# Kernel optimization log

Hardware: AMD Instinct MI355X
Metric: run time of the kernel (lower is better)

## Reference

```python
import jax, jax.numpy as jnp
import numpy as np

B, C, D, H, W = 2, 256, 4, 32, 32


def setup_inputs() -> dict:
    key = jax.random.key(0)
    k1, k2, k3, k4, k5 = jax.random.split(key, 5)
    s = 1.0 / np.sqrt(C)
    return {
        "exemplar_features": jax.random.normal(k1, (B, C, D, H, W), jnp.float32),
        "query_features": jax.random.normal(k2, (B, C, D, H, W), jnp.float32),
        "W_ex": jax.random.normal(k3, (C, C), jnp.float32) * s,    # nn.Linear weight (out,in)
        "W_q": jax.random.normal(k4, (C, C), jnp.float32) * s,     # nn.Linear weight (out,in)
        "W_gate": jax.random.normal(k5, (1, C, 1, 1, 1), jnp.float32) * s,  # Conv3d 1x1x1 weight
    }


def reference(exemplar_features, query_features, W_ex, W_q, W_gate):
    b, c, d, h, w = query_features.shape
    n = d * h * w
    ex = exemplar_features.reshape(b, c, n)   # (B,C,N)
    q = query_features.reshape(b, c, n)       # (B,C,N)
    ex_t = jnp.swapaxes(ex, 1, 2)              # (B,N,C)
    q_t = jnp.swapaxes(q, 1, 2)                # (B,N,C)
    # nn.Linear(no bias): x @ W.T
    ex_corr = jnp.einsum('bnc,dc->bnd', ex_t, W_ex)   # (B,N,C)
    q_corr = jnp.einsum('bnc,dc->bnd', q_t, W_q)      # (B,N,C)
    corr_e2q = jnp.einsum('bnc,bcm->bnm', ex_corr, q)  # (B,N,N)
    corr_q2e = jnp.einsum('bnc,bcm->bnm', q_corr, ex)  # (B,N,N)
    # softmax(transpose(corr,1,2), dim=1)
    A_e2q = jax.nn.softmax(jnp.swapaxes(corr_e2q, 1, 2), axis=1)  # (B,N,N)
    A_q2e = jax.nn.softmax(jnp.swapaxes(corr_q2e, 1, 2), axis=1)  # (B,N,N)
    ex_att = jnp.einsum('bcn,bnm->bcm', ex, A_e2q).reshape(b, c, d, h, w)
    q_att = jnp.einsum('bcn,bnm->bcm', q, A_q2e).reshape(b, c, d, h, w)
    # 1x1x1 Conv3d (256 -> 1, no bias) is a channel contraction
    g = W_gate[:, :, 0, 0, 0]  # (1,C)
    ex_mask = jax.nn.sigmoid(jnp.einsum('oc,bcdhw->bodhw', g, ex_att))
    q_mask = jax.nn.sigmoid(jnp.einsum('oc,bcdhw->bodhw', g, q_att))
    return ex_mask, q_mask, A_e2q, A_q2e
```

## Files before the change

kernel.cpp:

```cpp
#include <hip/hip_runtime.h>
#include <math.h>

#define BSZ  2
#define CDIM 256
#define NDIM 4096
#define SHIFT 110.0f

typedef _Float16 f16;
typedef f16  f16x8 __attribute__((ext_vector_type(8)));
typedef float f32x4 __attribute__((ext_vector_type(4)));

static const size_t F16N   = (size_t)BSZ * NDIM * CDIM;
static const size_t WS_FB  = 3 * F16N / 2;

__device__ __forceinline__ void gl_lds16(const void* g, void* l) {
    __builtin_amdgcn_global_load_lds(
        (const __attribute__((address_space(1))) void*)g,
        (__attribute__((address_space(3))) void*)l, 16, 0, 0);
}

__global__ __launch_bounds__(256) void corr_kernel(
    const float* __restrict__ ex, const float* __restrict__ q,
    const float* __restrict__ W_ex, const float* __restrict__ W_q,
    f16* __restrict__ Ah_e, f16* __restrict__ Al_e,
    f16* __restrict__ Ah_q, f16* __restrict__ Al_q)
{
    const int z   = blockIdx.z;
    const int sel = z >> 1;
    const int b   = z & 1;
    const float* feat = sel ? q   : ex;
    const float* W    = sel ? W_q : W_ex;
    f16* Ah = sel ? Ah_q : Ah_e;
    f16* Al = sel ? Al_q : Al_e;

    const int m0  = blockIdx.x * 128;
    const int cc0 = blockIdx.y * 128;
    const int t   = threadIdx.x;
    const int tx  = t & 15;
    const int ty  = t >> 4;

    __shared__ float sA[8][128];
    __shared__ float sB[8][128];

    float acc[8][8];
#pragma unroll
    for (int i = 0; i < 8; i++)
#pragma unroll
        for (int j = 0; j < 8; j++) acc[i][j] = 0.f;

    for (int k0 = 0; k0 < CDIM; k0 += 8) {
        {
            int kk = t >> 5, mi = (t & 31) * 4;
            *(float4*)(&sA[kk][mi]) =
                *(const float4*)(feat + ((size_t)(b * CDIM + k0 + kk)) * NDIM + m0 + mi);
        }
        {
            int ccj = t >> 1, kkb = (t & 1) * 4;
            float4 f = *(const float4*)(W + (size_t)(cc0 + ccj) * CDIM + k0 + kkb);
            sB[kkb + 0][ccj] = f.x; sB[kkb + 1][ccj] = f.y;
            sB[kkb + 2][ccj] = f.z; sB[kkb + 3][ccj] = f.w;
        }
        __syncthreads();
#pragma unroll
        for (int kk = 0; kk < 8; kk++) {
            float a[8], bb[8];
            *(float4*)(a)      = *(const float4*)(&sA[kk][ty * 8]);
            *(float4*)(a + 4)  = *(const float4*)(&sA[kk][ty * 8 + 4]);
            *(float4*)(bb)     = *(const float4*)(&sB[kk][tx * 8]);
            *(float4*)(bb + 4) = *(const float4*)(&sB[kk][tx * 8 + 4]);
#pragma unroll
            for (int i = 0; i < 8; i++)
#pragma unroll
                for (int j = 0; j < 8; j++)
                    acc[i][j] = fmaf(a[i], bb[j], acc[i][j]);
        }
        __syncthreads();
    }
#pragma unroll
    for (int i = 0; i < 8; i++) {
        const int m = m0 + ty * 8 + i;
        f16x8 hv, lv;
#pragma unroll
        for (int j = 0; j < 8; j++) {
            float x = acc[i][j];
            f16 hh = (f16)x;
            hv[j] = hh;
            lv[j] = (f16)(x - (float)hh);
        }
        const size_t off = ((size_t)(b * NDIM + m)) * CDIM + cc0 + tx * 8;
        *(f16x8*)(Ah + off) = hv;
        *(f16x8*)(Al + off) = lv;
    }
}

__global__ __launch_bounds__(256) void pack_b_kernel(
    const float* __restrict__ ex, const float* __restrict__ q,
    f16* __restrict__ Bq, f16* __restrict__ Bex)
{
    const int z   = blockIdx.z;
    const int sel = z >> 1;
    const int b   = z & 1;
    const float* feat = sel ? ex : q;
    f16* outp         = sel ? Bex : Bq;

    const int n0 = blockIdx.x * 64, c0 = blockIdx.y * 64;
    __shared__ float sT[64][65];
    const int t = threadIdx.x;
    const int tn = t & 63, tr = t >> 6;
#pragma unroll
    for (int r = 0; r < 16; ++r) {
        int c = tr + r * 4;
        sT[c][tn] = feat[((size_t)(b * CDIM + c0 + c)) * NDIM + n0 + tn];
    }
    __syncthreads();
#pragma unroll
    for (int r = 0; r < 16; ++r) {
        int n = tr + r * 4;
        outp[((size_t)(b * NDIM + n0 + n)) * CDIM + c0 + tn] = (f16)sT[tn][n];
    }
}

__global__ __launch_bounds__(256) void v_kernel(
    const float* __restrict__ ex, const float* __restrict__ q,
    const float* __restrict__ g,
    float* __restrict__ v_ex, float* __restrict__ v_q)
{
    __shared__ float sg[CDIM];
    const int t = threadIdx.x;
    sg[t] = g[t];
    __syncthreads();

    const int sel = blockIdx.z;
    const int b   = blockIdx.y;
    const float* feat = sel ? q : ex;
    float* outp       = sel ? v_q : v_ex;

    const int n = blockIdx.x * 256 + t;
    float acc = 0.f;
    for (int c = 0; c < CDIM; c++)
        acc = fmaf(sg[c], feat[((size_t)(b * CDIM + c)) * NDIM + n], acc);
    outp[b * NDIM + n] = acc;
}

__global__ __launch_bounds__(256) void score_mfma_kernel(
    const f16* __restrict__ Ah, const f16* __restrict__ Al,
    const f16* __restrict__ Bp, const float* __restrict__ v,
    float* __restrict__ outU,
    float* __restrict__ rowsum, float* __restrict__ rowdot)
{
    const int bb = blockIdx.z;
    const int m0 = blockIdx.x * 128;
    const int n0 = blockIdx.y * 128;
    const int t    = threadIdx.x;
    const int lane = t & 63;
    const int wv   = t >> 6;
    const int lq   = lane >> 4;
    const int ll   = lane & 15;

    __shared__ f16 sAh[8][128][8];
    __shared__ f16 sAl[8][128][8];
    __shared__ f16 sB [8][128][8];

    f32x4 acc[2][8];
#pragma unroll
    for (int mf = 0; mf < 2; mf++)
#pragma unroll
        for (int nf = 0; nf < 8; nf++) acc[mf][nf] = (f32x4)0.f;

    for (int k0 = 0; k0 < CDIM; k0 += 64) {
        if (k0) __syncthreads();
#pragma unroll
        for (int it = 0; it < 4; ++it) {
            const int cidx = (wv * 4 + it) * 64 + lane;
            const int kb = cidx >> 7;
            const int rr = cidx & 127;
            const size_t gA = ((size_t)(bb * NDIM + m0 + rr)) * CDIM + k0 + kb * 8;
            const size_t gB = ((size_t)(bb * NDIM + n0 + rr)) * CDIM + k0 + kb * 8;
            gl_lds16(Ah + gA, (char*)sAh + (size_t)cidx * 16);
            gl_lds16(Al + gA, (char*)sAl + (size_t)cidx * 16);
            gl_lds16(Bp + gB, (char*)sB  + (size_t)cidx * 16);
        }
        __syncthreads();
#pragma unroll
        for (int s = 0; s < 2; ++s) {
            f16x8 bfr[8];
#pragma unroll
            for (int nf = 0; nf < 8; ++nf)
                bfr[nf] = *(const f16x8*)&sB[4 * s + lq][nf * 16 + ll][0];
#pragma unroll
            for (int mf = 0; mf < 2; ++mf) {
                f16x8 ah = *(const f16x8*)&sAh[4 * s + lq][wv * 32 + mf * 16 + ll][0];
                f16x8 al = *(const f16x8*)&sAl[4 * s + lq][wv * 32 + mf * 16 + ll][0];
#pragma unroll
                for (int nf = 0; nf < 8; ++nf) {
                    acc[mf][nf] = __builtin_amdgcn_mfma_f32_16x16x32_f16(ah, bfr[nf], acc[mf][nf], 0, 0, 0);
                    acc[mf][nf] = __builtin_amdgcn_mfma_f32_16x16x32_f16(al, bfr[nf], acc[mf][nf], 0, 0, 0);
                }
            }
        }
    }

    float vv[8];
#pragma unroll
    for (int nf = 0; nf < 8; ++nf) vv[nf] = v[bb * NDIM + n0 + nf * 16 + ll];

    float rs[2][4], rd[2][4];
#pragma unroll
    for (int mf = 0; mf < 2; mf++)
#pragma unroll
        for (int r = 0; r < 4; r++) { rs[mf][r] = 0.f; rd[mf][r] = 0.f; }

#pragma unroll
    for (int mf = 0; mf < 2; ++mf) {
        const int mbase = m0 + wv * 32 + mf * 16 + lq * 4;
#pragma unroll
        for (int nf = 0; nf < 8; ++nf) {
            const int n = n0 + nf * 16 + ll;
            float4 u;
            u.x = __expf(acc[mf][nf][0] - SHIFT);
            u.y = __expf(acc[mf][nf][1] - SHIFT);
            u.z = __expf(acc[mf][nf][2] - SHIFT);
            u.w = __expf(acc[mf][nf][3] - SHIFT);
            *(float4*)(outU + ((size_t)(bb * NDIM + n)) * NDIM + mbase) = u;
            rs[mf][0] += u.x; rs[mf][1] += u.y; rs[mf][2] += u.z; rs[mf][3] += u.w;
            rd[mf][0] += u.x * vv[nf]; rd[mf][1] += u.y * vv[nf];
            rd[mf][2] += u.z * vv[nf]; rd[mf][3] += u.w * vv[nf];
        }
    }
#pragma unroll
    for (int mf = 0; mf < 2; ++mf) {
#pragma unroll
        for (int r = 0; r < 4; ++r) {
#pragma unroll
            for (int off = 1; off < 16; off <<= 1) {
                rs[mf][r] += __shfl_xor(rs[mf][r], off);
                rd[mf][r] += __shfl_xor(rd[mf][r], off);
            }
        }
        if (ll == 0) {
            const int mbase = m0 + wv * 32 + mf * 16 + lq * 4;
#pragma unroll
            for (int r = 0; r < 4; ++r) {
                atomicAdd(rowsum + bb * NDIM + mbase + r, rs[mf][r]);
                atomicAdd(rowdot + bb * NDIM + mbase + r, rd[mf][r]);
            }
        }
    }
}

__global__ __launch_bounds__(256) void mask_kernel(
    const float* __restrict__ sum_e, const float* __restrict__ dot_e,
    const float* __restrict__ sum_q, const float* __restrict__ dot_q,
    float* __restrict__ inv_e, float* __restrict__ inv_q,
    float* __restrict__ outp)
{
    const int idx = blockIdx.x * 256 + threadIdx.x;
    const int j = idx >> 13, i = idx & 8191;
    const float* s = j ? sum_q : sum_e;
    const float* d = j ? dot_q : dot_e;
    float* inv     = j ? inv_q : inv_e;
    const float sv = s[i];
    const float iv = 1.0f / sv;
    inv[i] = iv;
    const float x = d[i] * iv;
    outp[idx] = 1.0f / (1.0f + __expf(-x));
}

__global__ __launch_bounds__(256) void rescale_kernel(
    float* __restrict__ A, const float* __restrict__ inv)
{
    const size_t total4 = (size_t)BSZ * NDIM * NDIM / 4;
    const size_t stride = (size_t)gridDim.x * 256;
    for (size_t i4 = (size_t)blockIdx.x * 256 + threadIdx.x; i4 < total4; i4 += stride) {
        const size_t f = i4 * 4;
        const int m = (int)(f & (NDIM - 1));
        const int b = (int)(f >> 24);
        float4 u  = *(float4*)(A + f);
        float4 iv = *(const float4*)(inv + b * NDIM + m);
        u.x *= iv.x; u.y *= iv.y; u.z *= iv.z; u.w *= iv.w;
        *(float4*)(A + f) = u;
    }
}

extern "C" void kernel_launch(void* const* d_in, const int* in_sizes, int n_in,
                              void* d_out, int out_size, void* d_ws, size_t ws_size,
                              hipStream_t stream)
{
    const float* ex   = (const float*)d_in[0];
    const float* q    = (const float*)d_in[1];
    const float* W_ex = (const float*)d_in[2];
    const float* W_q  = (const float*)d_in[3];
    const float* g    = (const float*)d_in[4];
    float* outp = (float*)d_out;

    float* A_e2q = outp + 16384;
    float* A_q2e = A_e2q + (size_t)BSZ * NDIM * NDIM;

    f16* Ah_e = (f16*)A_q2e;
    f16* Al_e = Ah_e + F16N;
    f16* Bq   = Al_e + F16N;

    f16* Ah_q = (f16*)d_ws;
    f16* Al_q = Ah_q + F16N;
    f16* Bex  = Al_q + F16N;
    float* wsf  = (float*)d_ws + WS_FB;
    float* v_ex = wsf;
    float* v_q  = wsf + 8192;
    float* sum_e = wsf + 2 * 8192;
    float* dot_e = wsf + 3 * 8192;
    float* sum_q = wsf + 4 * 8192;
    float* dot_q = wsf + 5 * 8192;
    float* inv_e = wsf + 6 * 8192;
    float* inv_q = wsf + 7 * 8192;

    hipMemsetAsync(sum_e, 0, 4 * 8192 * sizeof(float), stream);

    corr_kernel<<<dim3(NDIM / 128, CDIM / 128, 2 * BSZ), 256, 0, stream>>>(
        ex, q, W_ex, W_q, Ah_e, Al_e, Ah_q, Al_q);

    pack_b_kernel<<<dim3(NDIM / 64, CDIM / 64, 2 * BSZ), 256, 0, stream>>>(
        ex, q, Bq, Bex);

    v_kernel<<<dim3(NDIM / 256, BSZ, 2), 256, 0, stream>>>(ex, q, g, v_ex, v_q);

    score_mfma_kernel<<<dim3(32, 32, BSZ), 256, 0, stream>>>(
        Ah_e, Al_e, Bq, v_ex, A_e2q, sum_e, dot_e);
    score_mfma_kernel<<<dim3(32, 32, BSZ), 256, 0, stream>>>(
        Ah_q, Al_q, Bex, v_q, A_q2e, sum_q, dot_q);

    mask_kernel<<<64, 256, 0, stream>>>(sum_e, dot_e, sum_q, dot_q, inv_e, inv_q, outp);

    rescale_kernel<<<32768, 256, 0, stream>>>(A_e2q, inv_e);
    rescale_kernel<<<32768, 256, 0, stream>>>(A_q2e, inv_q);
}
```

Baseline: 562.6 us.

## Fuse softmax normalization into score kernel via two-pass recompute

Replaces the tiled score GEMM plus atomics, mask kernel and two full-matrix rescale passes with one kernel per direction. Each block owns 16 rows: a first pass computes row sums and gate dot products, and a second pass recomputes the scores and writes normalized probabilities directly. This removes a full read-modify-write of both 128MB attention matrices, the memset and the atomics. In exchange it doubles the MFMA work and loads operands straight from global memory into registers instead of staging them in LDS, on a grid of only 512 blocks.

```diff
diff --git a/kernel.cpp b/kernel.cpp
--- a/kernel.cpp
+++ b/kernel.cpp
@@ -12,12 +12,6 @@
 
 static const size_t F16N   = (size_t)BSZ * NDIM * CDIM;
 static const size_t WS_FB  = 3 * F16N / 2;
-
-__device__ __forceinline__ void gl_lds16(const void* g, void* l) {
-    __builtin_amdgcn_global_load_lds(
-        (const __attribute__((address_space(1))) void*)g,
-        (__attribute__((address_space(3))) void*)l, 16, 0, 0);
-}
 
 __global__ __launch_bounds__(256) void corr_kernel(
     const float* __restrict__ ex, const float* __restrict__ q,
@@ -142,144 +136,131 @@
     outp[b * NDIM + n] = acc;
 }
 
-__global__ __launch_bounds__(256) void score_mfma_kernel(
+__global__ __launch_bounds__(256, 2) void flash_score_kernel(
     const f16* __restrict__ Ah, const f16* __restrict__ Al,
     const f16* __restrict__ Bp, const float* __restrict__ v,
-    float* __restrict__ outU,
-    float* __restrict__ rowsum, float* __restrict__ rowdot)
-{
-    const int bb = blockIdx.z;
-    const int m0 = blockIdx.x * 128;
-    const int n0 = blockIdx.y * 128;
-    const int t    = threadIdx.x;
-    const int lane = t & 63;
-    const int wv   = t >> 6;
-    const int lq   = lane >> 4;
-    const int ll   = lane & 15;
-
-    __shared__ f16 sAh[8][128][8];
-    __shared__ f16 sAl[8][128][8];
-    __shared__ f16 sB [8][128][8];
-
-    f32x4 acc[2][8];
-#pragma unroll
-    for (int mf = 0; mf < 2; mf++)
-#pragma unroll
-        for (int nf = 0; nf < 8; nf++) acc[mf][nf] = (f32x4)0.f;
-
-    for (int k0 = 0; k0 < CDIM; k0 += 64) {
-        if (k0) __syncthreads();
-#pragma unroll
-        for (int it = 0; it < 4; ++it) {
-            const int cidx = (wv * 4 + it) * 64 + lane;
-            const int kb = cidx >> 7;
-            const int rr = cidx & 127;
-            const size_t gA = ((size_t)(bb * NDIM + m0 + rr)) * CDIM + k0 + kb * 8;
-            const size_t gB = ((size_t)(bb * NDIM + n0 + rr)) * CDIM + k0 + kb * 8;
-            gl_lds16(Ah + gA, (char*)sAh + (size_t)cidx * 16);
-            gl_lds16(Al + gA, (char*)sAl + (size_t)cidx * 16);
-            gl_lds16(Bp + gB, (char*)sB  + (size_t)cidx * 16);
-        }
-        __syncthreads();
-#pragma unroll
-        for (int s = 0; s < 2; ++s) {
-            f16x8 bfr[8];
-#pragma unroll
-            for (int nf = 0; nf < 8; ++nf)
-                bfr[nf] = *(const f16x8*)&sB[4 * s + lq][nf * 16 + ll][0];
-#pragma unroll
-            for (int mf = 0; mf < 2; ++mf) {
-                f16x8 ah = *(const f16x8*)&sAh[4 * s + lq][wv * 32 + mf * 16 + ll][0];
-                f16x8 al = *(const f16x8*)&sAl[4 * s + lq][wv * 32 + mf * 16 + ll][0];
-#pragma unroll
-                for (int nf = 0; nf < 8; ++nf) {
-                    acc[mf][nf] = __builtin_amdgcn_mfma_f32_16x16x32_f16(ah, bfr[nf], acc[mf][nf], 0, 0, 0);
-                    acc[mf][nf] = __builtin_amdgcn_mfma_f32_16x16x32_f16(al, bfr[nf], acc[mf][nf], 0, 0, 0);
-                }
-            }
-        }
-    }
-
-    float vv[8];
-#pragma unroll
-    for (int nf = 0; nf < 8; ++nf) vv[nf] = v[bb * NDIM + n0 + nf * 16 + ll];
-
-    float rs[2][4], rd[2][4];
-#pragma unroll
-    for (int mf = 0; mf < 2; mf++)
-#pragma unroll
-        for (int r = 0; r < 4; r++) { rs[mf][r] = 0.f; rd[mf][r] = 0.f; }
-
-#pragma unroll
-    for (int mf = 0; mf < 2; ++mf) {
-        const int mbase = m0 + wv * 32 + mf * 16 + lq * 4;
-#pragma unroll
-        for (int nf = 0; nf < 8; ++nf) {
-            const int n = n0 + nf * 16 + ll;
-            float4 u;
-            u.x = __expf(acc[mf][nf][0] - SHIFT);
-            u.y = __expf(acc[mf][nf][1] - SHIFT);
-            u.z = __expf(acc[mf][nf][2] - SHIFT);
-            u.w = __expf(acc[mf][nf][3] - SHIFT);
-            *(float4*)(outU + ((size_t)(bb * NDIM + n)) * NDIM + mbase) = u;
-            rs[mf][0] += u.x; rs[mf][1] += u.y; rs[mf][2] += u.z; rs[mf][3] += u.w;
-            rd[mf][0] += u.x * vv[nf]; rd[mf][1] += u.y * vv[nf];
-            rd[mf][2] += u.z * vv[nf]; rd[mf][3] += u.w * vv[nf];
-        }
-    }
-#pragma unroll
-    for (int mf = 0; mf < 2; ++mf) {
+    float* __restrict__ outA, float* __restrict__ outMask)
+{
+    const int bb = blockIdx.y;
+    const int x  = blockIdx.x;
+    const int gpair = ((x >> 4) << 3) + (x & 7);
+    const int m0 = (gpair * 2 + ((x >> 3) & 1)) * 16;
+
+    const int t = threadIdx.x, lane = t & 63, wv = t >> 6;
+    const int lq = lane >> 4, ll = lane & 15;
+
+    const size_t aoff = ((size_t)(bb * NDIM + m0 + ll)) * CDIM + lq * 8;
+    f16x8 ah[8], al[8];
+#pragma unroll
+    for (int s = 0; s < 8; ++s) {
+        ah[s] = *(const f16x8*)(Ah + aoff + s * 32);
+        al[s] = *(const f16x8*)(Al + aoff + s * 32);
+    }
+
+    const f16*   bpw = Bp + ((size_t)(bb * NDIM + wv * 1024 + ll)) * CDIM + lq * 8;
+    const float* vp  = v + bb * NDIM + wv * 1024 + ll;
+    float*       outw = outA + ((size_t)(bb * NDIM + wv * 1024 + ll)) * NDIM + m0 + lq * 4;
+
+    f16x8 bx[16], by[16];
+    float rs[4] = {0.f, 0.f, 0.f, 0.f}, rd[4] = {0.f, 0.f, 0.f, 0.f};
+    float iv[4];
+
+#define LOADP(buf_, nf_) do {                                                 \
+        const f16* _p0 = bpw + (size_t)(nf_) * 16 * CDIM;                     \
+        const f16* _p1 = _p0 + 16 * CDIM;                                     \
+        _Pragma("unroll")                                                     \
+        for (int _s = 0; _s < 8; ++_s) {                                      \
+            buf_[_s]     = *(const f16x8*)(_p0 + _s * 32);                    \
+            buf_[8 + _s] = *(const f16x8*)(_p1 + _s * 32);                    \
+        } } while (0)
+
+#define MF(buf_, a0_, a1_) do {                                               \
+        _Pragma("unroll")                                                     \
+        for (int _s = 0; _s < 8; ++_s) {                                      \
+            a0_ = __builtin_amdgcn_mfma_f32_16x16x32_f16(ah[_s], buf_[_s],     a0_, 0, 0, 0); \
+            a0_ = __builtin_amdgcn_mfma_f32_16x16x32_f16(al[_s], buf_[_s],     a0_, 0, 0, 0); \
+            a1_ = __builtin_amdgcn_mfma_f32_16x16x32_f16(ah[_s], buf_[8 + _s], a1_, 0, 0, 0); \
+            a1_ = __builtin_amdgcn_mfma_f32_16x16x32_f16(al[_s], buf_[8 + _s], a1_, 0, 0, 0); \
+        } } while (0)
+
+#define CSUM(buf_, nf_) do {                                                  \
+        f32x4 _a0 = (f32x4)0.f, _a1 = (f32x4)0.f;                             \
+        MF(buf_, _a0, _a1);                                                   \
+        const float _v0 = vp[(nf_) * 16], _v1 = vp[(nf_) * 16 + 16];          \
+        _Pragma("unroll")                                                     \
+        for (int _r = 0; _r < 4; ++_r) {                                      \
+            const float _u0 = __expf(_a0[_r] - SHIFT);                        \
+            const float _u1 = __expf(_a1[_r] - SHIFT);                        \
+            rs[_r] += _u0 + _u1;                                              \
+            rd[_r] += _u0 * _v0 + _u1 * _v1;                                  \
+        } } while (0)
+
+#define CST(buf_, nf_) do {                                                   \
+        f32x4 _a0 = (f32x4)0.f, _a1 = (f32x4)0.f;                             \
+        MF(buf_, _a0, _a1);                                                   \
+        float4 _u;                                                            \
+        _u.x = __expf(_a0[0] - SHIFT) * iv[0];                                \
+        _u.y = __expf(_a0[1] - SHIFT) * iv[1];                                \
+        _u.z = __expf(_a0[2] - SHIFT) * iv[2];                                \
+        _u.w = __expf(_a0[3] - SHIFT) * iv[3];                                \
+        *(float4*)(outw + (size_t)(nf_) * 16 * NDIM) = _u;                    \
+        _u.x = __expf(_a1[0] - SHIFT) * iv[0];                                \
+        _u.y = __expf(_a1[1] - SHIFT) * iv[1];                                \
+        _u.z = __expf(_a1[2] - SHIFT) * iv[2];                                \
+        _u.w = __expf(_a1[3] - SHIFT) * iv[3];                                \
+        *(float4*)(outw + (size_t)(nf_ + 1) * 16 * NDIM) = _u;                \
+    } while (0)
+
+    LOADP(bx, 0);
+#pragma unroll 1
+    for (int nf = 0; nf < 64; nf += 4) {
+        LOADP(by, nf + 2);
+        CSUM(bx, nf);
+        if (nf + 4 < 64) LOADP(bx, nf + 4);
+        CSUM(by, nf + 2);
+    }
+
+#pragma unroll
+    for (int r = 0; r < 4; ++r)
+#pragma unroll
+        for (int off = 1; off < 16; off <<= 1) {
+            rs[r] += __shfl_xor(rs[r], off);
+            rd[r] += __shfl_xor(rd[r], off);
+        }
+
+    __shared__ float redS[4][4][4], redD[4][4][4];
+    if (ll == 0)
+#pragma unroll
+        for (int r = 0; r < 4; ++r) { redS[wv][lq][r] = rs[r]; redD[wv][lq][r] = rd[r]; }
+    __syncthreads();
+
+#pragma unroll
+    for (int r = 0; r < 4; ++r) {
+        const float ssum = redS[0][lq][r] + redS[1][lq][r] + redS[2][lq][r] + redS[3][lq][r];
+        iv[r] = 1.0f / ssum;
+    }
+    if (wv == 0 && ll == 0) {
 #pragma unroll
         for (int r = 0; r < 4; ++r) {
-#pragma unroll
-            for (int off = 1; off < 16; off <<= 1) {
-                rs[mf][r] += __shfl_xor(rs[mf][r], off);
-                rd[mf][r] += __shfl_xor(rd[mf][r], off);
-            }
-        }
-        if (ll == 0) {
-            const int mbase = m0 + wv * 32 + mf * 16 + lq * 4;
-#pragma unroll
-            for (int r = 0; r < 4; ++r) {
-                atomicAdd(rowsum + bb * NDIM + mbase + r, rs[mf][r]);
-                atomicAdd(rowdot + bb * NDIM + mbase + r, rd[mf][r]);
-            }
-        }
-    }
-}
-
-__global__ __launch_bounds__(256) void mask_kernel(
-    const float* __restrict__ sum_e, const float* __restrict__ dot_e,
-    const float* __restrict__ sum_q, const float* __restrict__ dot_q,
-    float* __restrict__ inv_e, float* __restrict__ inv_q,
-    float* __restrict__ outp)
-{
-    const int idx = blockIdx.x * 256 + threadIdx.x;
-    const int j = idx >> 13, i = idx & 8191;
-    const float* s = j ? sum_q : sum_e;
-    const float* d = j ? dot_q : dot_e;
-    float* inv     = j ? inv_q : inv_e;
-    const float sv = s[i];
-    const float iv = 1.0f / sv;
-    inv[i] = iv;
-    const float x = d[i] * iv;
-    outp[idx] = 1.0f / (1.0f + __expf(-x));
-}
-
-__global__ __launch_bounds__(256) void rescale_kernel(
-    float* __restrict__ A, const float* __restrict__ inv)
-{
-    const size_t total4 = (size_t)BSZ * NDIM * NDIM / 4;
-    const size_t stride = (size_t)gridDim.x * 256;
-    for (size_t i4 = (size_t)blockIdx.x * 256 + threadIdx.x; i4 < total4; i4 += stride) {
-        const size_t f = i4 * 4;
-        const int m = (int)(f & (NDIM - 1));
-        const int b = (int)(f >> 24);
-        float4 u  = *(float4*)(A + f);
-        float4 iv = *(const float4*)(inv + b * NDIM + m);
-        u.x *= iv.x; u.y *= iv.y; u.z *= iv.z; u.w *= iv.w;
-        *(float4*)(A + f) = u;
-    }
+            const float dsum = redD[0][lq][r] + redD[1][lq][r] + redD[2][lq][r] + redD[3][lq][r];
+            const float xx = dsum * iv[r];
+            outMask[bb * NDIM + m0 + lq * 4 + r] = 1.0f / (1.0f + __expf(-xx));
+        }
+    }
+
+    LOADP(bx, 0);
+#pragma unroll 1
+    for (int nf = 0; nf < 64; nf += 4) {
+        LOADP(by, nf + 2);
+        CST(bx, nf);
+        if (nf + 4 < 64) LOADP(bx, nf + 4);
+        CST(by, nf + 2);
+    }
+
+#undef LOADP
+#undef MF
+#undef CSUM
+#undef CST
 }
 
 extern "C" void kernel_launch(void* const* d_in, const int* in_sizes, int n_in,
@@ -306,14 +287,6 @@
     float* wsf  = (float*)d_ws + WS_FB;
     float* v_ex = wsf;
     float* v_q  = wsf + 8192;
-    float* sum_e = wsf + 2 * 8192;
-    float* dot_e = wsf + 3 * 8192;
-    float* sum_q = wsf + 4 * 8192;
-    float* dot_q = wsf + 5 * 8192;
-    float* inv_e = wsf + 6 * 8192;
-    float* inv_q = wsf + 7 * 8192;
-
-    hipMemsetAsync(sum_e, 0, 4 * 8192 * sizeof(float), stream);
 
     corr_kernel<<<dim3(NDIM / 128, CDIM / 128, 2 * BSZ), 256, 0, stream>>>(
         ex, q, W_ex, W_q, Ah_e, Al_e, Ah_q, Al_q);
@@ -323,13 +296,8 @@
 
     v_kernel<<<dim3(NDIM / 256, BSZ, 2), 256, 0, stream>>>(ex, q, g, v_ex, v_q);
 
-    score_mfma_kernel<<<dim3(32, 32, BSZ), 256, 0, stream>>>(
-        Ah_e, Al_e, Bq, v_ex, A_e2q, sum_e, dot_e);
-    score_mfma_kernel<<<dim3(32, 32, BSZ), 256, 0, stream>>>(
-        Ah_q, Al_q, Bex, v_q, A_q2e, sum_q, dot_q);
-
-    mask_kernel<<<64, 256, 0, stream>>>(sum_e, dot_e, sum_q, dot_q, inv_e, inv_q, outp);
-
-    rescale_kernel<<<32768, 256, 0, stream>>>(A_e2q, inv_e);
-    rescale_kernel<<<32768, 256, 0, stream>>>(A_q2e, inv_q);
-}
+    flash_score_kernel<<<dim3(256, BSZ), 256, 0, stream>>>(
+        Ah_e, Al_e, Bq, v_ex, A_e2q, outp);
+    flash_score_kernel<<<dim3(256, BSZ), 256, 0, stream>>>(
+        Ah_q, Al_q, Bex, v_q, A_q2e, outp + 8192);
+}
```

New measurement: 774.8 us. 1.38x slower.
